# Optimization experiments

Hardware: AMD Instinct MI355X
Metric: run time of the kernel (lower is better)

Reference implementation:

```python
import jax, jax.numpy as jnp
import numpy as np
import math

B, L, C_IN, D, H, FACTOR = 32, 512, 32, 512, 8, 1
E = D // H
TOP_K = int(FACTOR * math.log(L))  # 6


def setup_inputs() -> dict:
    key = jax.random.key(0)
    ks = jax.random.split(key, 14)
    s = 0.02
    f = lambda k, shp: jax.random.normal(k, shp, jnp.float32) * s
    return {
        "x": jax.random.normal(ks[0], (B, L, C_IN), jnp.float32),
        "conv_w": f(ks[1], (D, C_IN)),  # Conv1d kernel_size=1 == pointwise linear
        "conv_b": f(ks[2], (D,)),
        "wq": f(ks[3], (D, D)), "bq": f(ks[4], (D,)),
        "wk": f(ks[5], (D, D)), "bk": f(ks[6], (D,)),
        "wv": f(ks[7], (D, D)), "bv": f(ks[8], (D,)),
        "wo": f(ks[9], (D, D)), "bo": f(ks[10], (D,)),
        "lin_w": f(ks[11], (1, D)), "lin_b": f(ks[12], (1,)),
    }


def _autocorrelation(q, k, v):
    # q, k, v: [B, L, H, E]; Autoformer AutoCorrelation (inference delay agg)
    qf = jnp.fft.rfft(q.transpose(0, 2, 3, 1), axis=-1)        # [B,H,E,Lf]
    kf = jnp.fft.rfft(k.transpose(0, 2, 3, 1), axis=-1)
    corr = jnp.fft.irfft(qf * jnp.conj(kf), n=L, axis=-1)       # [B,H,E,L]
    vals = v.transpose(0, 2, 3, 1)                              # [B,H,E,L]
    mean_corr = corr.mean(axis=(1, 2))                          # [B,L]
    weights, delay = jax.lax.top_k(mean_corr, TOP_K)            # [B,k]
    w = jax.nn.softmax(weights, axis=-1)                        # [B,k]
    # gather values at (t + delay) mod L  (== doubled-values trick in torch)
    idx = (jnp.arange(L)[None, None, :] + delay[:, :, None]) % L  # [B,k,L]
    patterns = jnp.take_along_axis(
        vals[:, :, :, None, :], idx[:, None, None, :, :], axis=-1)  # [B,H,E,k,L]
    agg = jnp.einsum('bhekl,bk->bhel', patterns, w)             # [B,H,E,L]
    return agg.transpose(0, 3, 1, 2)                            # [B,L,H,E]


def reference(x, conv_w, conv_b, wq, bq, wk, bk, wv, bv, wo, bo, lin_w, lin_b):
    # pointwise conv1d projection: [B,L,C_IN] -> [B,L,D]
    h = x @ conv_w.T + conv_b
    q = (h @ wq.T + bq).reshape(B, L, H, E)
    k = (h @ wk.T + bk).reshape(B, L, H, E)
    v = (h @ wv.T + bv).reshape(B, L, H, E)
    attn_out = _autocorrelation(q, k, v).reshape(B, L, D)
    new_x = attn_out @ wo.T + bo
    out = h + new_x          # residual
    last = out[:, -1:, :]    # x[:, -1:]
    y = last @ lin_w.T + lin_b  # [B,1,1]
    return y
```

## Files before the change

kernel.cpp:

```cpp
#include <hip/hip_runtime.h>
#include <hip/hip_bf16.h>

#define LL 512
#define BB 32
#define DD 512
#define CINN 32
#define TOPK 6
#define BL (BB * LL)

typedef __attribute__((ext_vector_type(8))) short bf16x8;
typedef __attribute__((ext_vector_type(4))) float f32x4;

__device__ inline float bf2f(ushort u) {
    union { uint i; float f; } c; c.i = ((uint)u) << 16; return c.f;
}
__device__ inline ushort f2bf(float f) {
    union { float f; uint i; } c; c.f = f;
    uint i = c.i;
    return (ushort)((i + 0x7FFFu + ((i >> 16) & 1u)) >> 16);
}
__device__ inline void split_bf(float v, ushort& hi, ushort& lo) {
    hi = f2bf(v);
    lo = f2bf(v - bf2f(hi));
}
__device__ inline uint pk2(ushort a, ushort b) { return (uint)a | ((uint)b << 16); }

__device__ inline bf16x8 frag_ld(const ushort* sm, int r, int s) {
    return *(const bf16x8*)(sm + r * 32 + ((s ^ ((r >> 1) & 3)) << 3));
}

__device__ inline void mfma_step(const ushort* sAh, const ushort* sAl,
                                 const ushort* sBh, const ushort* sBl,
                                 f32x4 acc[4][4], int wr, int wc, int fr, int fs) {
    bf16x8 bh[4], blo[4];
    #pragma unroll
    for (int ni = 0; ni < 4; ++ni) {
        bh[ni]  = frag_ld(sBh, wc + ni * 16 + fr, fs);
        blo[ni] = frag_ld(sBl, wc + ni * 16 + fr, fs);
    }
    #pragma unroll
    for (int mi = 0; mi < 4; ++mi) {
        const bf16x8 ah = frag_ld(sAh, wr + mi * 16 + fr, fs);
        const bf16x8 al = frag_ld(sAl, wr + mi * 16 + fr, fs);
        #pragma unroll
        for (int ni = 0; ni < 4; ++ni) {
            acc[mi][ni] = __builtin_amdgcn_mfma_f32_16x16x32_bf16(ah, bh[ni],  acc[mi][ni], 0, 0, 0);
            acc[mi][ni] = __builtin_amdgcn_mfma_f32_16x16x32_bf16(ah, blo[ni], acc[mi][ni], 0, 0, 0);
            acc[mi][ni] = __builtin_amdgcn_mfma_f32_16x16x32_bf16(al, bh[ni],  acc[mi][ni], 0, 0, 0);
        }
    }
}

__global__ __launch_bounds__(256) void prep_kernel(
    const float* __restrict__ wq, const float* __restrict__ wk,
    const float* __restrict__ cw,
    const float* __restrict__ lin_w, const float* __restrict__ wo,
    const float* __restrict__ wv,
    float* __restrict__ Mpart, float* __restrict__ ug,
    float* __restrict__ v2g, float* __restrict__ mc)
{
    const int tid = threadIdx.x;
    if (blockIdx.x < 64) {
        __shared__ float cws[512][32];
        __shared__ float wqsT[512][9];
        __shared__ float wksT[512][9];
        __shared__ float aqs[8][32];
        __shared__ float aks[8][32];
        if (blockIdx.x < 32) {
            mc[blockIdx.x * 512 + tid] = 0.f;
            mc[blockIdx.x * 512 + tid + 256] = 0.f;
        }
        for (int i = tid; i < 4096; i += 256) {
            const int d = i >> 3, q = i & 7;
            *(float4*)&cws[d][q * 4] = *(const float4*)(cw + (long)d * 32 + q * 4);
        }
        const int e0 = blockIdx.x * 8;
        for (int i = tid; i < 4096; i += 256) {
            const int e = i >> 9, d = i & 511;
            wqsT[d][e] = wq[(long)(e0 + e) * 512 + d];
            wksT[d][e] = wk[(long)(e0 + e) * 512 + d];
        }
        __syncthreads();
        const int e_loc = tid >> 5, c = tid & 31;
        float aq = 0.f, ak = 0.f;
        #pragma unroll 4
        for (int d = 0; d < 512; ++d) {
            const float cv = cws[d][c];
            aq += wqsT[d][e_loc] * cv;
            ak += wksT[d][e_loc] * cv;
        }
        aqs[e_loc][c] = aq;
        aks[e_loc][c] = ak;
        __syncthreads();
        const int c_ = tid >> 3, cq = tid & 7;
        float m0 = 0.f, m1 = 0.f, m2 = 0.f, m3 = 0.f;
        #pragma unroll
        for (int e = 0; e < 8; ++e) {
            const float a = aqs[e][c_];
            const float4 k4 = *(const float4*)&aks[e][cq * 4];
            m0 += a * k4.x; m1 += a * k4.y; m2 += a * k4.z; m3 += a * k4.w;
        }
        *(float4*)(Mpart + (long)blockIdx.x * 1024 + c_ * 32 + cq * 4) =
            make_float4(m0, m1, m2, m3);
    } else {
        __shared__ float us[512];
        float u0 = 0.f, u1 = 0.f;
        for (int n = 0; n < 512; ++n) {
            const float lw = lin_w[n];
            u0 += lw * wo[(long)n * 512 + tid];
            u1 += lw * wo[(long)n * 512 + tid + 256];
        }
        us[tid] = u0; us[tid + 256] = u1;
        ug[tid] = u0; ug[tid + 256] = u1;
        __syncthreads();
        float s0 = 0.f, s1 = 0.f;
        for (int d = 0; d < 512; ++d) {
            const float ud = us[d];
            s0 += ud * wv[(long)d * 512 + tid];
            s1 += ud * wv[(long)d * 512 + tid + 256];
        }
        v2g[tid] = s0; v2g[tid + 256] = s1;
    }
}

__global__ __launch_bounds__(256, 2) void corr_kernel(
    const float* __restrict__ x, const float* __restrict__ Mpart,
    float* __restrict__ mc)
{
    __shared__ ushort buf[16384];
    __shared__ float Ml[32][36];
    __shared__ float mcloc[LL];
    ushort* bufAh = buf;
    ushort* bufAl = buf + 4096;
    ushort* bufBh = buf + 8192;
    ushort* bufBl = buf + 12288;
    const int tid = threadIdx.x;

    const int xcd = blockIdx.x & 7, s = blockIdx.x >> 3;
    const int b = xcd * 4 + (s >> 4);
    const int tile = s & 15;
    const int tm = tile >> 2, tn = tile & 3;

    {
        float4 ms = make_float4(0.f, 0.f, 0.f, 0.f);
        for (int p = 0; p < 64; ++p) {
            const float4 v = *(const float4*)(Mpart + (long)p * 1024 + tid * 4);
            ms.x += v.x; ms.y += v.y; ms.z += v.z; ms.w += v.w;
        }
        *(float4*)&Ml[tid >> 3][(tid & 7) * 4] = ms;
    }
    mcloc[tid] = 0.f; mcloc[tid + 256] = 0.f;

    const int r = tid >> 1;
    const int pb = (tid & 1) * 2;
    const int swz = (r >> 1) & 3;
    const float* xA = x + ((long)b * LL + tm * 128 + r) * 32;
    const float* xB = x + ((long)b * LL + tn * 128 + r) * 32;
    float xb[32];
    #pragma unroll
    for (int q = 0; q < 8; ++q)
        *(float4*)&xb[q * 4] = *(const float4*)(xB + q * 4);

    __syncthreads();

    #pragma unroll
    for (int pi = 0; pi < 2; ++pi) {
        const int p = pb + pi;
        const int sl = p ^ swz;
        const int uoff = (r * 4 + p) * 8;
        const float4 a0 = *(const float4*)(xA + sl * 8);
        const float4 a1 = *(const float4*)(xA + sl * 8 + 4);
        const float xe[8] = {a0.x, a0.y, a0.z, a0.w, a1.x, a1.y, a1.z, a1.w};
        ushort xh[8], xl[8];
        #pragma unroll
        for (int j = 0; j < 8; ++j) split_bf(xe[j], xh[j], xl[j]);
        *(uint4*)(bufAh + uoff) = make_uint4(pk2(xh[0], xh[1]), pk2(xh[2], xh[3]),
                                             pk2(xh[4], xh[5]), pk2(xh[6], xh[7]));
        *(uint4*)(bufAl + uoff) = make_uint4(pk2(xl[0], xl[1]), pk2(xl[2], xl[3]),
                                             pk2(xl[4], xl[5]), pk2(xl[6], xl[7]));
        float uv[8];
        #pragma unroll
        for (int j = 0; j < 8; ++j) {
            const int c = sl * 8 + j;
            float sacc = 0.f;
            #pragma unroll
            for (int q = 0; q < 8; ++q) {
                const float4 m = *(const float4*)&Ml[c][q * 4];
                sacc += m.x * xb[q * 4] + m.y * xb[q * 4 + 1]
                      + m.z * xb[q * 4 + 2] + m.w * xb[q * 4 + 3];
            }
            uv[j] = sacc;
        }
        ushort uh[8], ul[8];
        #pragma unroll
        for (int j = 0; j < 8; ++j) split_bf(uv[j], uh[j], ul[j]);
        *(uint4*)(bufBh + uoff) = make_uint4(pk2(uh[0], uh[1]), pk2(uh[2], uh[3]),
                                             pk2(uh[4], uh[5]), pk2(uh[6], uh[7]));
        *(uint4*)(bufBl + uoff) = make_uint4(pk2(ul[0], ul[1]), pk2(ul[2], ul[3]),
                                             pk2(ul[4], ul[5]), pk2(ul[6], ul[7]));
    }
    __syncthreads();

    {
        const int wid = tid >> 6, lane = tid & 63;
        const int wr = (wid >> 1) * 64, wc = (wid & 1) * 64;
        const int fr = lane & 15, fs = lane >> 4;
        f32x4 acc[4][4] = {};
        mfma_step(bufAh, bufAl, bufBh, bufBl, acc, wr, wc, fr, fs);

        const int base = wr - wc + 128 * (tm - tn) + fs * 4 - fr;
        #pragma unroll
        for (int k = -3; k <= 3; ++k) {
            #pragma unroll
            for (int rr = 0; rr < 4; ++rr) {
                float sdg = 0.f;
                #pragma unroll
                for (int mi = 0; mi < 4; ++mi) {
                    const int ni = mi - k;
                    if (ni >= 0 && ni < 4) sdg += acc[mi][ni][rr];
                }
                atomicAdd(&mcloc[(base + 16 * k + rr) & (LL - 1)], sdg);
            }
        }
    }
    __syncthreads();
    atomicAdd(&mc[b * 512 + tid], mcloc[tid]);
    atomicAdd(&mc[b * 512 + tid + 256], mcloc[tid + 256]);
}

__global__ __launch_bounds__(256) void tail_kernel(
    const float* __restrict__ mc, const float* __restrict__ x,
    const float* __restrict__ ug, const float* __restrict__ v2g,
    const float* __restrict__ cw, const float* __restrict__ cb,
    const float* __restrict__ lin_w, const float* __restrict__ bv,
    const float* __restrict__ bo, const float* __restrict__ lin_b,
    float* __restrict__ out)
{
    const int b = blockIdx.x, tid = threadIdx.x;
    const int lane = tid & 63, wid = tid >> 6;
    __shared__ float v2s[512];
    __shared__ float us2[512];
    __shared__ float w3p[8][32];
    __shared__ float w4p[8][32];
    __shared__ float w3s[32];
    __shared__ float w4s[32];
    __shared__ float c2s;
    __shared__ float swv[4];
    __shared__ int   swi[4];
    __shared__ float selv[TOPK];
    __shared__ int   seli[TOPK];
    __shared__ float wts[TOPK];
    __shared__ float redc[4];

    v2s[tid] = v2g[tid]; v2s[tid + 256] = v2g[tid + 256];
    us2[tid] = ug[tid];  us2[tid + 256] = ug[tid + 256];
    __syncthreads();
    {
        const int c = tid & 31, g = tid >> 5;
        float w3 = 0.f, w4 = 0.f;
        for (int dl = 0; dl < 64; ++dl) {
            const int d = g * 64 + dl;
            const float cwv = cw[(long)d * 32 + c];
            w3 += v2s[d] * cwv;
            w4 += lin_w[d] * cwv;
        }
        w3p[g][c] = w3; w4p[g][c] = w4;
    }
    __syncthreads();
    if (tid < 32) {
        float a3 = 0.f, a4 = 0.f;
        #pragma unroll
        for (int g2 = 0; g2 < 8; ++g2) { a3 += w3p[g2][tid]; a4 += w4p[g2][tid]; }
        w3s[tid] = a3; w4s[tid] = a4;
    }
    {
        float p = cb[tid] * (v2s[tid] + lin_w[tid])
                + cb[tid + 256] * (v2s[tid + 256] + lin_w[tid + 256])
                + bv[tid] * us2[tid] + bv[tid + 256] * us2[tid + 256]
                + bo[tid] * lin_w[tid] + bo[tid + 256] * lin_w[tid + 256];
        #pragma unroll
        for (int o = 32; o; o >>= 1) p += __shfl_down(p, o);
        if ((tid & 63) == 0) redc[tid >> 6] = p;
    }
    __syncthreads();
    if (tid == 0) c2s = redc[0] + redc[1] + redc[2] + redc[3] + lin_b[0];

    float v0 = mc[b * 512 + tid] * (1.0f / DD);
    float v1 = mc[b * 512 + tid + 256] * (1.0f / DD);

    int live0 = 1, live1 = 1;
    for (int r = 0; r < TOPK; ++r) {
        float bvv = -1e30f; int bi = -1;
        if (live0) { bvv = v0; bi = tid; }
        if (live1 && v1 > bvv) { bvv = v1; bi = tid + 256; }
        #pragma unroll
        for (int o = 32; o; o >>= 1) {
            const float ov = __shfl_down(bvv, o);
            const int oi = __shfl_down(bi, o);
            if (ov > bvv || (ov == bvv && oi < bi)) { bvv = ov; bi = oi; }
        }
        if (lane == 0) { swv[wid] = bvv; swi[wid] = bi; }
        __syncthreads();
        if (tid == 0) {
            float fv = swv[0]; int fi = swi[0];
            #pragma unroll
            for (int w2 = 1; w2 < 4; ++w2) {
                if (swv[w2] > fv || (swv[w2] == fv && swi[w2] < fi)) { fv = swv[w2]; fi = swi[w2]; }
            }
            selv[r] = fv; seli[r] = fi;
        }
        __syncthreads();
        const int w = seli[r];
        if (w == tid)       live0 = 0;
        if (w == tid + 256) live1 = 0;
    }
    if (tid == 0) {
        const float mx = selv[0];
        float e[TOPK], ssum = 0.f;
        #pragma unroll
        for (int k = 0; k < TOPK; ++k) { e[k] = expf(selv[k] - mx); ssum += e[k]; }
        #pragma unroll
        for (int k = 0; k < TOPK; ++k) wts[k] = e[k] / ssum;
    }
    __syncthreads();

    if (tid < CINN) {
        float xm = 0.f;
        #pragma unroll
        for (int k = 0; k < TOPK; ++k) {
            const int r = (LL - 1 + seli[k]) & (LL - 1);
            xm += wts[k] * x[((long)b * LL + r) * CINN + tid];
        }
        const float xlv = x[((long)b * LL + (LL - 1)) * CINN + tid];
        float yv = xlv * w4s[tid] + xm * w3s[tid];
        #pragma unroll
        for (int o = 16; o; o >>= 1) yv += __shfl_down(yv, o);
        if (tid == 0) out[b] = yv + c2s;
    }
}

extern "C" void kernel_launch(void* const* d_in, const int* in_sizes, int n_in,
                              void* d_out, int out_size, void* d_ws, size_t ws_size,
                              hipStream_t stream) {
    const float* x      = (const float*)d_in[0];
    const float* conv_w = (const float*)d_in[1];
    const float* conv_b = (const float*)d_in[2];
    const float* wq     = (const float*)d_in[3];
    const float* wk     = (const float*)d_in[5];
    const float* wv     = (const float*)d_in[7];
    const float* bv     = (const float*)d_in[8];
    const float* wo     = (const float*)d_in[9];
    const float* bo     = (const float*)d_in[10];
    const float* lin_w  = (const float*)d_in[11];
    const float* lin_b  = (const float*)d_in[12];

    char* w = (char*)d_ws;
    float* Mpart = (float*)w;  w += (long)64 * 1024 * 4;
    float* ug    = (float*)w;  w += 512 * 4;
    float* v2g   = (float*)w;  w += 512 * 4;
    float* mc    = (float*)w;  w += (long)BB * 512 * 4;
    float* yout  = (float*)d_out;

    prep_kernel<<<65, 256, 0, stream>>>(wq, wk, conv_w, lin_w, wo, wv,
                                        Mpart, ug, v2g, mc);
    corr_kernel<<<512, 256, 0, stream>>>(x, Mpart, mc);
    tail_kernel<<<BB, 256, 0, stream>>>(mc, x, ug, v2g,
                                        conv_w, conv_b, lin_w, bv, bo, lin_b, yout);
}
```

Measured before the change: 70.11 us.

## Split serial weight-folding block into parallel blocks and precompute Wv·Wc

Previously a single prep block serially computed u = lin_w·Wo and then v2 = u·Wv, two dependent 512x512 matvecs, which likely bounded prep latency. Now the u computation is split across 8 blocks as partial sums. Wv is folded with the conv weight inside the existing 64 blocks, and Wv·cb and lin_w·cw are computed in separate blocks. The tail kernel reduces the partial u vectors and applies the folded 512x32 matrix per batch. This shortens the critical path at the cost of redundant per-batch work in the tail and an extra wv load in the 64 blocks.

```diff
diff --git a/kernel.cpp b/kernel.cpp
--- a/kernel.cpp
+++ b/kernel.cpp
@@ -53,17 +53,19 @@
 
 __global__ __launch_bounds__(256) void prep_kernel(
     const float* __restrict__ wq, const float* __restrict__ wk,
-    const float* __restrict__ cw,
+    const float* __restrict__ wv, const float* __restrict__ cw,
+    const float* __restrict__ cb,
     const float* __restrict__ lin_w, const float* __restrict__ wo,
-    const float* __restrict__ wv,
-    float* __restrict__ Mpart, float* __restrict__ ug,
-    float* __restrict__ v2g, float* __restrict__ mc)
+    float* __restrict__ Mpart, float* __restrict__ upart,
+    float* __restrict__ Wvc, float* __restrict__ wvcb,
+    float* __restrict__ w4g, float* __restrict__ mc)
 {
     const int tid = threadIdx.x;
     if (blockIdx.x < 64) {
         __shared__ float cws[512][32];
         __shared__ float wqsT[512][9];
         __shared__ float wksT[512][9];
+        __shared__ float wvsT[512][9];
         __shared__ float aqs[8][32];
         __shared__ float aks[8][32];
         if (blockIdx.x < 32) {
@@ -79,18 +81,21 @@
             const int e = i >> 9, d = i & 511;
             wqsT[d][e] = wq[(long)(e0 + e) * 512 + d];
             wksT[d][e] = wk[(long)(e0 + e) * 512 + d];
+            wvsT[d][e] = wv[(long)(e0 + e) * 512 + d];
         }
         __syncthreads();
         const int e_loc = tid >> 5, c = tid & 31;
-        float aq = 0.f, ak = 0.f;
+        float aq = 0.f, ak = 0.f, av = 0.f;
         #pragma unroll 4
         for (int d = 0; d < 512; ++d) {
             const float cv = cws[d][c];
             aq += wqsT[d][e_loc] * cv;
             ak += wksT[d][e_loc] * cv;
+            av += wvsT[d][e_loc] * cv;
         }
         aqs[e_loc][c] = aq;
         aks[e_loc][c] = ak;
+        Wvc[(long)(e0 + e_loc) * 32 + c] = av;
         __syncthreads();
         const int c_ = tid >> 3, cq = tid & 7;
         float m0 = 0.f, m1 = 0.f, m2 = 0.f, m3 = 0.f;
@@ -102,24 +107,41 @@
         }
         *(float4*)(Mpart + (long)blockIdx.x * 1024 + c_ * 32 + cq * 4) =
             make_float4(m0, m1, m2, m3);
+    } else if (blockIdx.x < 72) {
+        const int j = blockIdx.x - 64;
+        const int n0 = j * 64;
+        float u0 = 0.f, u1 = 0.f;
+        for (int n = 0; n < 64; ++n) {
+            const float lw = lin_w[n0 + n];
+            u0 += lw * wo[(long)(n0 + n) * 512 + tid];
+            u1 += lw * wo[(long)(n0 + n) * 512 + tid + 256];
+        }
+        upart[j * 512 + tid] = u0;
+        upart[j * 512 + tid + 256] = u1;
+        const int e = j * 64 + (tid >> 2);
+        const int q = tid & 3;
+        float p = 0.f;
+        const float* wvr = wv + (long)e * 512 + q * 128;
+        for (int dl = 0; dl < 128; ++dl) p += wvr[dl] * cb[q * 128 + dl];
+        p += __shfl_xor(p, 1);
+        p += __shfl_xor(p, 2);
+        if (q == 0) wvcb[e] = p;
     } else {
-        __shared__ float us[512];
-        float u0 = 0.f, u1 = 0.f;
-        for (int n = 0; n < 512; ++n) {
-            const float lw = lin_w[n];
-            u0 += lw * wo[(long)n * 512 + tid];
-            u1 += lw * wo[(long)n * 512 + tid + 256];
-        }
-        us[tid] = u0; us[tid + 256] = u1;
-        ug[tid] = u0; ug[tid + 256] = u1;
-        __syncthreads();
-        float s0 = 0.f, s1 = 0.f;
-        for (int d = 0; d < 512; ++d) {
-            const float ud = us[d];
-            s0 += ud * wv[(long)d * 512 + tid];
-            s1 += ud * wv[(long)d * 512 + tid + 256];
-        }
-        v2g[tid] = s0; v2g[tid + 256] = s1;
+        __shared__ float w4p[8][32];
+        const int g = tid >> 5, c = tid & 31;
+        float p = 0.f;
+        for (int dl = 0; dl < 64; ++dl) {
+            const int d = g * 64 + dl;
+            p += lin_w[d] * cw[(long)d * 32 + c];
+        }
+        w4p[g][c] = p;
+        __syncthreads();
+        if (tid < 32) {
+            float s = 0.f;
+            #pragma unroll
+            for (int g2 = 0; g2 < 8; ++g2) s += w4p[g2][tid];
+            w4g[tid] = s;
+        }
     }
 }
 
@@ -230,18 +252,17 @@
 
 __global__ __launch_bounds__(256) void tail_kernel(
     const float* __restrict__ mc, const float* __restrict__ x,
-    const float* __restrict__ ug, const float* __restrict__ v2g,
-    const float* __restrict__ cw, const float* __restrict__ cb,
-    const float* __restrict__ lin_w, const float* __restrict__ bv,
-    const float* __restrict__ bo, const float* __restrict__ lin_b,
+    const float* __restrict__ upart, const float* __restrict__ Wvc,
+    const float* __restrict__ wvcb, const float* __restrict__ w4g,
+    const float* __restrict__ cb, const float* __restrict__ lin_w,
+    const float* __restrict__ bv, const float* __restrict__ bo,
+    const float* __restrict__ lin_b,
     float* __restrict__ out)
 {
     const int b = blockIdx.x, tid = threadIdx.x;
     const int lane = tid & 63, wid = tid >> 6;
-    __shared__ float v2s[512];
     __shared__ float us2[512];
     __shared__ float w3p[8][32];
-    __shared__ float w4p[8][32];
     __shared__ float w3s[32];
     __shared__ float w4s[32];
     __shared__ float c2s;
@@ -252,32 +273,38 @@
     __shared__ float wts[TOPK];
     __shared__ float redc[4];
 
-    v2s[tid] = v2g[tid]; v2s[tid + 256] = v2g[tid + 256];
-    us2[tid] = ug[tid];  us2[tid + 256] = ug[tid + 256];
-    __syncthreads();
-    {
-        const int c = tid & 31, g = tid >> 5;
-        float w3 = 0.f, w4 = 0.f;
-        for (int dl = 0; dl < 64; ++dl) {
-            const int d = g * 64 + dl;
-            const float cwv = cw[(long)d * 32 + c];
-            w3 += v2s[d] * cwv;
-            w4 += lin_w[d] * cwv;
-        }
-        w3p[g][c] = w3; w4p[g][c] = w4;
+    {
+        float b0 = 0.f, b1 = 0.f;
+        #pragma unroll
+        for (int i = 0; i < 8; ++i) {
+            b0 += upart[i * 512 + tid];
+            b1 += upart[i * 512 + tid + 256];
+        }
+        us2[tid] = b0; us2[tid + 256] = b1;
+    }
+    __syncthreads();
+    {
+        const int g = tid >> 5, c = tid & 31;
+        float p = 0.f;
+        for (int el = 0; el < 64; ++el) {
+            const int e = g * 64 + el;
+            p += us2[e] * Wvc[(long)e * 32 + c];
+        }
+        w3p[g][c] = p;
     }
     __syncthreads();
     if (tid < 32) {
-        float a3 = 0.f, a4 = 0.f;
-        #pragma unroll
-        for (int g2 = 0; g2 < 8; ++g2) { a3 += w3p[g2][tid]; a4 += w4p[g2][tid]; }
-        w3s[tid] = a3; w4s[tid] = a4;
-    }
-    {
-        float p = cb[tid] * (v2s[tid] + lin_w[tid])
-                + cb[tid + 256] * (v2s[tid + 256] + lin_w[tid + 256])
-                + bv[tid] * us2[tid] + bv[tid + 256] * us2[tid + 256]
-                + bo[tid] * lin_w[tid] + bo[tid + 256] * lin_w[tid + 256];
+        float s = 0.f;
+        #pragma unroll
+        for (int g2 = 0; g2 < 8; ++g2) s += w3p[g2][tid];
+        w3s[tid] = s;
+        w4s[tid] = w4g[tid];
+    }
+    {
+        float p = us2[tid] * (wvcb[tid] + bv[tid])
+                + us2[tid + 256] * (wvcb[tid + 256] + bv[tid + 256])
+                + lin_w[tid] * (cb[tid] + bo[tid])
+                + lin_w[tid + 256] * (cb[tid + 256] + bo[tid + 256]);
         #pragma unroll
         for (int o = 32; o; o >>= 1) p += __shfl_down(p, o);
         if ((tid & 63) == 0) redc[tid >> 6] = p;
@@ -356,14 +383,16 @@
 
     char* w = (char*)d_ws;
     float* Mpart = (float*)w;  w += (long)64 * 1024 * 4;
-    float* ug    = (float*)w;  w += 512 * 4;
-    float* v2g   = (float*)w;  w += 512 * 4;
+    float* upart = (float*)w;  w += (long)8 * 512 * 4;
+    float* Wvc   = (float*)w;  w += (long)512 * 32 * 4;
+    float* wvcb  = (float*)w;  w += 512 * 4;
+    float* w4g   = (float*)w;  w += 32 * 4;
     float* mc    = (float*)w;  w += (long)BB * 512 * 4;
     float* yout  = (float*)d_out;
 
-    prep_kernel<<<65, 256, 0, stream>>>(wq, wk, conv_w, lin_w, wo, wv,
-                                        Mpart, ug, v2g, mc);
+    prep_kernel<<<73, 256, 0, stream>>>(wq, wk, wv, conv_w, conv_b, lin_w, wo,
+                                        Mpart, upart, Wvc, wvcb, w4g, mc);
     corr_kernel<<<512, 256, 0, stream>>>(x, Mpart, mc);
-    tail_kernel<<<BB, 256, 0, stream>>>(mc, x, ug, v2g,
-                                        conv_w, conv_b, lin_w, bv, bo, lin_b, yout);
-}
+    tail_kernel<<<BB, 256, 0, stream>>>(mc, x, upart, Wvc, wvcb, w4g,
+                                        conv_b, lin_w, bv, bo, lin_b, yout);
+}
```

Measured after the change: 65.59 us. -6.4%, faster.
